# Kernel optimization log

Measured on AMD Instinct MI355X. Metric: run time of the kernel, lower is better.

## Reference

```python
import jax, jax.numpy as jnp
import numpy as np

DIM = 1024
NUM_HEADS = 16
DIM_HEAD = 64
INNER = NUM_HEADS * DIM_HEAD  # 1024
B, N = 2, 2048


def setup_inputs() -> dict:
    key = jax.random.key(0)
    k1, k2, k3 = jax.random.split(key, 3)
    x = jax.random.normal(k1, (B, N, DIM), dtype=jnp.float32)
    # nn.Linear(dim, inner*3, bias=False): weight [3*inner, dim]; y = x @ W^T
    w_qkv = jax.random.normal(k2, (3 * INNER, DIM), dtype=jnp.float32) * (DIM ** -0.5)
    # to_out: Linear(inner, dim) with bias
    w_out = jax.random.normal(k3, (DIM, INNER), dtype=jnp.float32) * (INNER ** -0.5)
    b_out = jnp.zeros((DIM,), dtype=jnp.float32)
    return {"x": x, "w_qkv": w_qkv, "w_out": w_out, "b_out": b_out}


def reference(x, w_qkv, w_out, b_out):
    b, n, d = x.shape
    scale = DIM_HEAD ** -0.5
    qkv = jnp.einsum('bnd,ed->bne', x, w_qkv)  # [b, n, 3*inner]
    q, k, v = jnp.split(qkv, 3, axis=-1)
    # [b, n, h, dh] -> [b, h, n, dh]
    reshape = lambda t: t.reshape(b, n, NUM_HEADS, DIM_HEAD).transpose(0, 2, 1, 3)
    q, k, v = reshape(q), reshape(k), reshape(v)
    dots = jnp.einsum('bhqd,bhkd->bhqk', q, k) * scale  # [b, h, n, n]
    attn = jax.nn.softmax(dots, axis=-1)
    out = jnp.einsum('bhqk,bhkd->bhqd', attn, v)
    out = out.transpose(0, 2, 1, 3).reshape(b, n, INNER)
    out = jnp.einsum('bni,oi->bno', out, w_out) + b_out
    return out
```

## Files before the change

kernel.cpp:

```cpp
#include <hip/hip_runtime.h>
#include <hip/hip_bf16.h>
#include <stdint.h>

typedef unsigned short u16;
typedef short bf16x8 __attribute__((ext_vector_type(8)));
typedef float f32x4 __attribute__((ext_vector_type(4)));
typedef float f32x16 __attribute__((ext_vector_type(16)));
typedef u16 u16x4 __attribute__((ext_vector_type(4)));
typedef unsigned int uint2v __attribute__((ext_vector_type(2)));

#define DIMX  1024
#define NHEAD 16
#define DH    64
#define INNER 1024
#define BATCH 2
#define SEQ   2048
#define MTOT  (BATCH*SEQ)
#define EQKV  (3*INNER)

__device__ __forceinline__ u16 f2bf(float f) {
  unsigned int x = __float_as_uint(f);
  unsigned int r = (x + 0x7FFFu + ((x >> 16) & 1u)) >> 16;
  return (u16)r;
}

__device__ __forceinline__ unsigned int cvtpk(float lo, float hi) {
  unsigned int r;
  asm("v_cvt_pk_bf16_f32 %0, %1, %2" : "=v"(r) : "v"(lo), "v"(hi));
  return r;
}

__device__ __forceinline__ void plswap_u(unsigned int& x, unsigned int& y) {
  auto r = __builtin_amdgcn_permlane32_swap(x, y, false, false);
  x = r[0]; y = r[1];
}
__device__ __forceinline__ void plswap_f2(float v, float& a, float& b) {
  unsigned int x = __float_as_uint(v), y = __float_as_uint(v);
  auto r = __builtin_amdgcn_permlane32_swap(x, y, false, false);
  a = __uint_as_float(r[0]); b = __uint_as_float(r[1]);
}

__device__ __forceinline__ void async16(void* lds, const void* g) {
  __builtin_amdgcn_global_load_lds(
      (const __attribute__((address_space(1))) unsigned int*)g,
      (__attribute__((address_space(3))) unsigned int*)lds,
      16, 0, 0);
}

__device__ __forceinline__ int swz4(int r) { return (r ^ (r >> 2)) & 3; }

#define X4C (MTOT * DIMX / 4)
#define W4C (EQKV * DIMX / 4)
#define O4C (DIMX * INNER / 4)
__global__ void cvt_all(const float* __restrict__ x, const float* __restrict__ wq,
                        const float* __restrict__ wo, u16* __restrict__ xb,
                        u16* __restrict__ wqb, u16* __restrict__ wob) {
  int i = blockIdx.x * blockDim.x + threadIdx.x;
  const float* src; u16* dst; int off;
  if (i < X4C)            { src = x;  dst = xb;  off = i; }
  else if (i < X4C + W4C) { src = wq; dst = wqb; off = i - X4C; }
  else                    { src = wo; dst = wob; off = i - X4C - W4C; }
  float4 v = ((const float4*)src)[off];
  u16x4 o;
  o[0] = f2bf(v.x); o[1] = f2bf(v.y); o[2] = f2bf(v.z); o[3] = f2bf(v.w);
  ((u16x4*)dst)[off] = o;
}

__global__ __launch_bounds__(256) void gemm_qkv(const u16* __restrict__ X, const u16* __restrict__ W,
                                                u16* __restrict__ Qo, u16* __restrict__ Ko,
                                                u16* __restrict__ Vt) {
  __shared__ short sAll[24576];
  short* sA = sAll;
  short* sB = sAll + 12288;
  const int tid = threadIdx.x;
  const int wv = tid >> 6, l = tid & 63;
  const int lo = l & 15, hi = l >> 4;
  const int wr = wv >> 1, wc = wv & 1;

  int lin = blockIdx.x;
  int wgid = (lin & 7) * 96 + (lin >> 3);
  const int bx = wgid / 32;
  const int by = wgid % 32;
  const int tn = bx * 128, tm = by * 128;

  f32x4 acc[4][4];
#pragma unroll
  for (int i = 0; i < 4; i++)
#pragma unroll
    for (int j = 0; j < 4; j++) acc[i][j] = (f32x4){0.f, 0.f, 0.f, 0.f};

  auto stageT = [&](int buf, int kt) {
    int k0 = kt * 32;
    int off = buf * 4096;
#pragma unroll
    for (int c = 0; c < 2; c++) {
      int R0 = wv * 32 + c * 16;
      int r = R0 + (l >> 2);
      int sc = ((l & 3) ^ swz4(r)) * 8;
      async16(&sA[off + R0 * 32], &X[(size_t)(tm + r) * DIMX + k0 + sc]);
      async16(&sB[off + R0 * 32], &W[(size_t)(tn + r) * DIMX + k0 + sc]);
    }
  };

  auto compute = [&](int buf) {
    bf16x8 af[4], bf[4];
#pragma unroll
    for (int i = 0; i < 4; i++) {
      int r = wr * 64 + i * 16 + lo;
      af[i] = *(const bf16x8*)&sA[buf * 4096 + r * 32 + ((hi ^ swz4(r)) * 8)];
    }
#pragma unroll
    for (int j = 0; j < 4; j++) {
      int r = wc * 64 + j * 16 + lo;
      bf[j] = *(const bf16x8*)&sB[buf * 4096 + r * 32 + ((hi ^ swz4(r)) * 8)];
    }
#pragma unroll
    for (int i = 0; i < 4; i++)
#pragma unroll
      for (int j = 0; j < 4; j++)
        acc[i][j] = __builtin_amdgcn_mfma_f32_16x16x32_bf16(af[i], bf[j], acc[i][j], 0, 0, 0);
  };

  const int NT = DIMX / 32;
  stageT(0, 0);
  stageT(1, 1);
  int bc = 0;
  for (int kt = 0; kt < NT - 2; kt++) {
    int bs = bc + 2; if (bs >= 3) bs -= 3;
    stageT(bs, kt + 2);
    asm volatile("s_waitcnt vmcnt(8)" ::: "memory");
    asm volatile("s_barrier" ::: "memory");
    __builtin_amdgcn_sched_barrier(0);
    compute(bc);
    __builtin_amdgcn_sched_barrier(0);
    asm volatile("s_barrier" ::: "memory");
    bc = (bc == 2) ? 0 : bc + 1;
  }
  asm volatile("s_waitcnt vmcnt(4)" ::: "memory");
  asm volatile("s_barrier" ::: "memory");
  __builtin_amdgcn_sched_barrier(0);
  compute(bc);
  __builtin_amdgcn_sched_barrier(0);
  asm volatile("s_barrier" ::: "memory");
  bc = (bc == 2) ? 0 : bc + 1;
  asm volatile("s_waitcnt vmcnt(0)" ::: "memory");
  asm volatile("s_barrier" ::: "memory");
  __builtin_amdgcn_sched_barrier(0);
  compute(bc);
  __builtin_amdgcn_sched_barrier(0);
  __syncthreads();

  const int cls = tn >> 10;
  const float scale = 0.125f * 1.44269504088896f;

  if (cls < 2) {
#pragma unroll
    for (int i = 0; i < 4; i++) {
      int mbase = tm + wr * 64 + i * 16 + hi * 4;
#pragma unroll
      for (int j = 0; j < 4; j++) {
        int e = tn + wc * 64 + j * 16 + lo;
        int e2 = e & 1023, h = e2 >> 6, d = e2 & 63;
        u16* base = (cls == 0) ? Qo : Ko;
        float s = (cls == 0) ? scale : 1.0f;
        size_t a0 = (((size_t)((mbase >> 11) * NHEAD + h)) * SEQ) * DH + d;
#pragma unroll
        for (int rp = 0; rp < 2; rp++) {
          int n0 = (mbase + rp * 2) & 2047;
          unsigned int pk = cvtpk(acc[i][j][rp * 2] * s, acc[i][j][rp * 2 + 1] * s);
          base[a0 + (size_t)n0 * DH] = (u16)pk;
          base[a0 + (size_t)(n0 + 1) * DH] = (u16)(pk >> 16);
        }
      }
    }
  } else {
#pragma unroll
    for (int i = 0; i < 4; i++) {
#pragma unroll
      for (int j = 0; j < 4; j++) {
        int e = wc * 64 + j * 16 + lo;
#pragma unroll
        for (int rp = 0; rp < 2; rp++) {
          int n = wr * 64 + i * 16 + hi * 4 + rp * 2;
          unsigned int pk = cvtpk(acc[i][j][rp * 2], acc[i][j][rp * 2 + 1]);
          *(unsigned int*)&sAll[e * 128 + (((n >> 3) ^ (e & 15)) * 8) + (n & 7)] = pk;
        }
      }
    }
    __syncthreads();
    int er = tid >> 1, half = tid & 1;
    int e2 = tn + er - 2048;
    int h = e2 >> 6, d = e2 & 63;
    int b = tm >> 11, nb = tm & 2047;
    u16* dst = &Vt[(((size_t)(b * NHEAD + h)) * DH + d) * SEQ + nb + half * 64];
#pragma unroll
    for (int k = 0; k < 8; k++) {
      int phys = (half * 8 + k) ^ (er & 15);
      bf16x8 v = *(const bf16x8*)&sAll[er * 128 + phys * 8];
      *(bf16x8*)&dst[k * 8] = v;
    }
  }
}

__global__ __launch_bounds__(256) void attn_kernel(const u16* __restrict__ Q, const u16* __restrict__ Kd,
                                                   const u16* __restrict__ Vt, u16* __restrict__ O) {
  __shared__ short sK[2][64 * 64];
  __shared__ short sV[2][64 * 64];
  const int tid = threadIdx.x, wv = tid >> 6, l = tid & 63;
  const int l31 = l & 31, hi5 = l >> 5, l7 = l & 7;

  int lin = blockIdx.y * gridDim.x + blockIdx.x;
  int wgid = (lin & 7) * 64 + (lin >> 3);
  int bx = wgid & 15;
  int bh = wgid >> 4;

  const int qw = bx * 128 + wv * 32;
  const u16* Qb = Q + (size_t)bh * SEQ * DH;
  const u16* Kb = Kd + (size_t)bh * SEQ * DH;
  const u16* Vb = Vt + (size_t)bh * DH * SEQ;

  bf16x8 qf[4];
#pragma unroll
  for (int kd = 0; kd < 4; kd++)
    qf[kd] = *(const bf16x8*)&Qb[(size_t)(qw + l31) * DH + kd * 16 + hi5 * 8];

  f32x16 o0, o1;
#pragma unroll
  for (int r = 0; r < 16; r++) { o0[r] = 0.f; o1[r] = 0.f; }
  float lsum = 0.f;
  const float CSHIFT = 12.0f;

  auto stage = [&](int buf, int t) {
    int kv0 = t * 64;
#pragma unroll
    for (int c = 0; c < 2; c++) {
      int rbase = wv * 16 + c * 8;
      int gr = rbase + (l >> 3);
      int sc = ((l & 7) ^ (l >> 3)) * 8;
      async16(&sK[buf][rbase * 64], &Kb[(size_t)(kv0 + gr) * DH + sc]);
      async16(&sV[buf][rbase * 64], &Vb[(size_t)gr * SEQ + kv0 + sc]);
    }
  };

  stage(0, 0);
  __syncthreads();

  for (int t = 0; t < SEQ / 64; t++) {
    const int cur = t & 1;
    if (t + 1 < SEQ / 64) stage(cur ^ 1, t + 1);

    bf16x8 kf0[4], kf1[4], vf0[4], vf1[4];
#pragma unroll
    for (int kd = 0; kd < 4; kd++) {
      int c16 = ((kd * 2 + hi5) ^ l7) * 8;
      kf0[kd] = *(const bf16x8*)&sK[cur][l31 * 64 + c16];
      kf1[kd] = *(const bf16x8*)&sK[cur][(32 + l31) * 64 + c16];
      vf0[kd] = *(const bf16x8*)&sV[cur][l31 * 64 + c16];
      vf1[kd] = *(const bf16x8*)&sV[cur][(32 + l31) * 64 + c16];
    }

    f32x16 s0, s1;
#pragma unroll
    for (int r = 0; r < 16; r++) { s0[r] = -CSHIFT; s1[r] = -CSHIFT; }
#pragma unroll
    for (int kd = 0; kd < 4; kd++) {
      s0 = __builtin_amdgcn_mfma_f32_32x32x16_bf16(kf0[kd], qf[kd], s0, 0, 0, 0);
      s1 = __builtin_amdgcn_mfma_f32_32x32x16_bf16(kf1[kd], qf[kd], s1, 0, 0, 0);
    }

    float sm[16];
#pragma unroll
    for (int r = 0; r < 16; r++) {
      s0[r] = __builtin_amdgcn_exp2f(s0[r]);
      s1[r] = __builtin_amdgcn_exp2f(s1[r]);
      sm[r] = s0[r] + s1[r];
    }
#pragma unroll
    for (int st = 8; st > 0; st >>= 1)
#pragma unroll
      for (int r = 0; r < st; r++) sm[r] += sm[r + st];
    lsum += sm[0];

    bf16x8 pa[4];
#pragma unroll
    for (int ks = 0; ks < 4; ks++) {
      const int sft = (ks & 1) * 8;
      float e0 = (ks < 2) ? s0[sft + 0] : s1[sft + 0];
      float e1 = (ks < 2) ? s0[sft + 1] : s1[sft + 1];
      float e2 = (ks < 2) ? s0[sft + 2] : s1[sft + 2];
      float e3 = (ks < 2) ? s0[sft + 3] : s1[sft + 3];
      float e4 = (ks < 2) ? s0[sft + 4] : s1[sft + 4];
      float e5 = (ks < 2) ? s0[sft + 5] : s1[sft + 5];
      float e6 = (ks < 2) ? s0[sft + 6] : s1[sft + 6];
      float e7 = (ks < 2) ? s0[sft + 7] : s1[sft + 7];
      unsigned int w0 = cvtpk(e0, e1);
      unsigned int w1 = cvtpk(e2, e3);
      unsigned int w2 = cvtpk(e4, e5);
      unsigned int w3 = cvtpk(e6, e7);
      plswap_u(w0, w2);
      plswap_u(w1, w3);
      union { unsigned int w[4]; bf16x8 v; } u;
      u.w[0] = w0; u.w[1] = w1; u.w[2] = w2; u.w[3] = w3;
      pa[ks] = u.v;
    }

#pragma unroll
    for (int ks = 0; ks < 4; ks++) {
      o0 = __builtin_amdgcn_mfma_f32_32x32x16_bf16(vf0[ks], pa[ks], o0, 0, 0, 0);
      o1 = __builtin_amdgcn_mfma_f32_32x32x16_bf16(vf1[ks], pa[ks], o1, 0, 0, 0);
    }
    __syncthreads();
  }

  float la, lb;
  plswap_f2(lsum, la, lb);
  float inv = 1.0f / (la + lb);

  int b = bh >> 4, h = bh & 15;
  int q = qw + l31;
  size_t orow = ((size_t)(b * SEQ + q)) * INNER + h * 64;
#pragma unroll
  for (int half = 0; half < 2; half++) {
    const f32x16& oo = half ? o1 : o0;
#pragma unroll
    for (int g = 0; g < 4; g++) {
      uint2v pk2;
      pk2[0] = cvtpk(oo[g * 4 + 0] * inv, oo[g * 4 + 1] * inv);
      pk2[1] = cvtpk(oo[g * 4 + 2] * inv, oo[g * 4 + 3] * inv);
      int dv = half * 32 + g * 8 + 4 * hi5;
      *(uint2v*)&O[orow + dv] = pk2;
    }
  }
}

__global__ __launch_bounds__(256) void gemm_out(const u16* __restrict__ A, const u16* __restrict__ W,
                                                const float* __restrict__ bias, float* __restrict__ out) {
  __shared__ short sAll[12288];
  short* sA = sAll;
  short* sB = sAll + 8192;
  const int tid = threadIdx.x;
  const int wv = tid >> 6, l = tid & 63;
  const int lo = l & 15, hi = l >> 4;
  const int wr = wv >> 1, wc = wv & 1;

  int lin = blockIdx.x;
  int wgid = (lin & 7) * 64 + (lin >> 3);
  const int bx = wgid / 32;
  const int by = wgid % 32;
  const int tn = bx * 64, tm = by * 128;

  f32x4 acc[4][2];
#pragma unroll
  for (int i = 0; i < 4; i++)
#pragma unroll
    for (int j = 0; j < 2; j++) acc[i][j] = (f32x4){0.f, 0.f, 0.f, 0.f};

  auto stage = [&](int buf, int kt) {
    int k0 = kt * 32;
#pragma unroll
    for (int c = 0; c < 2; c++) {
      int R0 = wv * 32 + c * 16;
      int r = R0 + (l >> 2);
      int sc = ((l & 3) ^ swz4(r)) * 8;
      async16(&sA[buf * 4096 + R0 * 32], &A[(size_t)(tm + r) * INNER + k0 + sc]);
    }
    int rB = wv * 16 + (l >> 2);
    int scB = ((l & 3) ^ swz4(rB)) * 8;
    async16(&sB[buf * 2048 + (wv * 16) * 32], &W[(size_t)(tn + rB) * INNER + k0 + scB]);
  };

  stage(0, 0);
  __syncthreads();

  for (int kt = 0; kt < INNER / 32; kt++) {
    const int buf = kt & 1;
    if (kt + 1 < INNER / 32) stage(buf ^ 1, kt + 1);
    bf16x8 af[4], bf[2];
#pragma unroll
    for (int i = 0; i < 4; i++) {
      int r = wr * 64 + i * 16 + lo;
      af[i] = *(const bf16x8*)&sA[buf * 4096 + r * 32 + ((hi ^ swz4(r)) * 8)];
    }
#pragma unroll
    for (int j = 0; j < 2; j++) {
      int r = wc * 32 + j * 16 + lo;
      bf[j] = *(const bf16x8*)&sB[buf * 2048 + r * 32 + ((hi ^ swz4(r)) * 8)];
    }
#pragma unroll
    for (int i = 0; i < 4; i++)
#pragma unroll
      for (int j = 0; j < 2; j++)
        acc[i][j] = __builtin_amdgcn_mfma_f32_16x16x32_bf16(af[i], bf[j], acc[i][j], 0, 0, 0);
    __syncthreads();
  }

#pragma unroll
  for (int i = 0; i < 4; i++) {
    int mbase = tm + wr * 64 + i * 16 + hi * 4;
#pragma unroll
    for (int j = 0; j < 2; j++) {
      int col = tn + wc * 32 + j * 16 + lo;
      float bv = bias[col];
#pragma unroll
      for (int r = 0; r < 4; r++)
        out[(size_t)(mbase + r) * DIMX + col] = acc[i][j][r] + bv;
    }
  }
}

extern "C" void kernel_launch(void* const* d_in, const int* in_sizes, int n_in,
                              void* d_out, int out_size, void* d_ws, size_t ws_size,
                              hipStream_t stream) {
  const float* x     = (const float*)d_in[0];
  const float* w_qkv = (const float*)d_in[1];
  const float* w_out = (const float*)d_in[2];
  const float* b_out = (const float*)d_in[3];

  char* ws = (char*)d_ws;
  u16* xb    = (u16*)(ws);
  u16* wqkvb = (u16*)(ws + (size_t)8  * (1<<20));
  u16* woutb = (u16*)(ws + (size_t)14 * (1<<20));
  u16* Qd    = (u16*)(ws + (size_t)16 * (1<<20));
  u16* Kdd   = (u16*)(ws + (size_t)24 * (1<<20));
  u16* Vtd   = (u16*)(ws + (size_t)32 * (1<<20));
  u16* Od    = (u16*)(ws + (size_t)40 * (1<<20));

  cvt_all<<<(X4C + W4C + O4C) / 256, 256, 0, stream>>>(x, w_qkv, w_out, xb, wqkvb, woutb);

  gemm_qkv<<<768, 256, 0, stream>>>(xb, wqkvb, Qd, Kdd, Vtd);
  attn_kernel<<<dim3(SEQ / 128, BATCH * NHEAD), 256, 0, stream>>>(Qd, Kdd, Vtd, Od);
  gemm_out<<<512, 256, 0, stream>>>(Od, woutb, b_out, (float*)d_out);
}
```

Before: 120.0 us.

## Pre-shuffle K/V into MFMA fragment layout and load directly to registers

The QKV projection epilogue now writes K and V in a layout that matches the per-lane MFMA operand order for each 64-row tile. The attention kernel then loads K and V fragments straight from global memory into registers, with K for the next tile prefetched into a ping-pong register set, instead of staging through LDS with barriers. This removes LDS traffic and the per-tile __syncthreads. In exchange, every wave reads K/V from global/L2 on its own, losing LDS sharing across the 4 waves, and register pressure rises.

```diff
diff --git a/kernel.cpp b/kernel.cpp
--- a/kernel.cpp
+++ b/kernel.cpp
@@ -17,6 +17,8 @@
 #define SEQ   2048
 #define MTOT  (BATCH*SEQ)
 #define EQKV  (3*INNER)
+#define HSTRIDE 131072
+#define TSTRIDE 4096
 
 __device__ __forceinline__ u16 f2bf(float f) {
   unsigned int x = __float_as_uint(f);
@@ -153,23 +155,44 @@
   const int cls = tn >> 10;
   const float scale = 0.125f * 1.44269504088896f;
 
-  if (cls < 2) {
+  if (cls == 0) {
 #pragma unroll
     for (int i = 0; i < 4; i++) {
       int mbase = tm + wr * 64 + i * 16 + hi * 4;
 #pragma unroll
       for (int j = 0; j < 4; j++) {
         int e = tn + wc * 64 + j * 16 + lo;
-        int e2 = e & 1023, h = e2 >> 6, d = e2 & 63;
-        u16* base = (cls == 0) ? Qo : Ko;
-        float s = (cls == 0) ? scale : 1.0f;
+        int h = e >> 6, d = e & 63;
         size_t a0 = (((size_t)((mbase >> 11) * NHEAD + h)) * SEQ) * DH + d;
 #pragma unroll
         for (int rp = 0; rp < 2; rp++) {
           int n0 = (mbase + rp * 2) & 2047;
-          unsigned int pk = cvtpk(acc[i][j][rp * 2] * s, acc[i][j][rp * 2 + 1] * s);
-          base[a0 + (size_t)n0 * DH] = (u16)pk;
-          base[a0 + (size_t)(n0 + 1) * DH] = (u16)(pk >> 16);
+          unsigned int pk = cvtpk(acc[i][j][rp * 2] * scale, acc[i][j][rp * 2 + 1] * scale);
+          Qo[a0 + (size_t)n0 * DH] = (u16)pk;
+          Qo[a0 + (size_t)(n0 + 1) * DH] = (u16)(pk >> 16);
+        }
+      }
+    }
+  } else if (cls == 1) {
+#pragma unroll
+    for (int i = 0; i < 4; i++) {
+      int mbase = tm + wr * 64 + i * 16 + hi * 4;
+      int b = mbase >> 11;
+#pragma unroll
+      for (int j = 0; j < 4; j++) {
+        int e2 = (tn + wc * 64 + j * 16 + lo) - 1024;
+        int h = e2 >> 6, d = e2 & 63;
+        int kd = d >> 4, hi5k = (d >> 3) & 1, e8 = d & 7;
+        size_t hb = (size_t)(b * NHEAD + h) * HSTRIDE + (size_t)kd * 512 + hi5k * 256 + e8;
+#pragma unroll
+        for (int rp = 0; rp < 2; rp++) {
+          int n0 = (mbase + rp * 2) & 2047;
+          int t_ = n0 >> 6, kvi = n0 & 63;
+          int c = kvi >> 5, l31k = kvi & 31;
+          unsigned int pk = cvtpk(acc[i][j][rp * 2], acc[i][j][rp * 2 + 1]);
+          size_t a = hb + (size_t)t_ * TSTRIDE + c * 2048 + l31k * 8;
+          Ko[a] = (u16)pk;
+          Ko[a + 8] = (u16)(pk >> 16);
         }
       }
     }
@@ -190,24 +213,25 @@
     __syncthreads();
     int er = tid >> 1, half = tid & 1;
     int e2 = tn + er - 2048;
-    int h = e2 >> 6, d = e2 & 63;
+    int h = e2 >> 6, dv = e2 & 63;
     int b = tm >> 11, nb = tm & 2047;
-    u16* dst = &Vt[(((size_t)(b * NHEAD + h)) * DH + d) * SEQ + nb + half * 64];
+    int c = dv >> 5, l31v = dv & 31;
+    size_t vb = (size_t)(b * NHEAD + h) * HSTRIDE
+              + (size_t)((nb >> 6) + half) * TSTRIDE + (size_t)c * 2048 + l31v * 8;
 #pragma unroll
     for (int k = 0; k < 8; k++) {
       int phys = (half * 8 + k) ^ (er & 15);
       bf16x8 v = *(const bf16x8*)&sAll[er * 128 + phys * 8];
-      *(bf16x8*)&dst[k * 8] = v;
-    }
-  }
-}
-
-__global__ __launch_bounds__(256) void attn_kernel(const u16* __restrict__ Q, const u16* __restrict__ Kd,
-                                                   const u16* __restrict__ Vt, u16* __restrict__ O) {
-  __shared__ short sK[2][64 * 64];
-  __shared__ short sV[2][64 * 64];
+      int ks = k >> 1, hi5v = k & 1;
+      *(bf16x8*)&Vt[vb + ks * 512 + hi5v * 256] = v;
+    }
+  }
+}
+
+__global__ __launch_bounds__(256) void attn_kernel(const u16* __restrict__ Q, const u16* __restrict__ Ksh,
+                                                   const u16* __restrict__ Vsh, u16* __restrict__ O) {
   const int tid = threadIdx.x, wv = tid >> 6, l = tid & 63;
-  const int l31 = l & 31, hi5 = l >> 5, l7 = l & 7;
+  const int l31 = l & 31, hi5 = l >> 5;
 
   int lin = blockIdx.y * gridDim.x + blockIdx.x;
   int wgid = (lin & 7) * 64 + (lin >> 3);
@@ -216,8 +240,8 @@
 
   const int qw = bx * 128 + wv * 32;
   const u16* Qb = Q + (size_t)bh * SEQ * DH;
-  const u16* Kb = Kd + (size_t)bh * SEQ * DH;
-  const u16* Vb = Vt + (size_t)bh * DH * SEQ;
+  const u16* Kb = Ksh + (size_t)bh * HSTRIDE + l * 8;
+  const u16* Vb = Vsh + (size_t)bh * HSTRIDE + l * 8;
 
   bf16x8 qf[4];
 #pragma unroll
@@ -230,42 +254,35 @@
   float lsum = 0.f;
   const float CSHIFT = 12.0f;
 
-  auto stage = [&](int buf, int t) {
-    int kv0 = t * 64;
-#pragma unroll
-    for (int c = 0; c < 2; c++) {
-      int rbase = wv * 16 + c * 8;
-      int gr = rbase + (l >> 3);
-      int sc = ((l & 7) ^ (l >> 3)) * 8;
-      async16(&sK[buf][rbase * 64], &Kb[(size_t)(kv0 + gr) * DH + sc]);
-      async16(&sV[buf][rbase * 64], &Vb[(size_t)gr * SEQ + kv0 + sc]);
+  bf16x8 kA0[4], kA1[4], kB0[4], kB1[4];
+
+  auto loadK = [&](bf16x8 (&k0)[4], bf16x8 (&k1)[4], int t) {
+    const u16* p = Kb + (size_t)t * TSTRIDE;
+#pragma unroll
+    for (int kd = 0; kd < 4; kd++) {
+      k0[kd] = *(const bf16x8*)&p[kd * 512];
+      k1[kd] = *(const bf16x8*)&p[2048 + kd * 512];
     }
   };
 
-  stage(0, 0);
-  __syncthreads();
-
-  for (int t = 0; t < SEQ / 64; t++) {
-    const int cur = t & 1;
-    if (t + 1 < SEQ / 64) stage(cur ^ 1, t + 1);
-
-    bf16x8 kf0[4], kf1[4], vf0[4], vf1[4];
+  auto tile = [&](bf16x8 (&kc0)[4], bf16x8 (&kc1)[4],
+                  bf16x8 (&kn0)[4], bf16x8 (&kn1)[4], int t) {
+    const u16* pv = Vb + (size_t)t * TSTRIDE;
+    bf16x8 vf0[4], vf1[4];
+#pragma unroll
+    for (int ks = 0; ks < 4; ks++) {
+      vf0[ks] = *(const bf16x8*)&pv[ks * 512];
+      vf1[ks] = *(const bf16x8*)&pv[2048 + ks * 512];
+    }
+    if (t + 1 < SEQ / 64) loadK(kn0, kn1, t + 1);
+
+    f32x16 s0, s1;
+#pragma unroll
+    for (int r = 0; r < 16; r++) { s0[r] = -CSHIFT; s1[r] = -CSHIFT; }
 #pragma unroll
     for (int kd = 0; kd < 4; kd++) {
-      int c16 = ((kd * 2 + hi5) ^ l7) * 8;
-      kf0[kd] = *(const bf16x8*)&sK[cur][l31 * 64 + c16];
-      kf1[kd] = *(const bf16x8*)&sK[cur][(32 + l31) * 64 + c16];
-      vf0[kd] = *(const bf16x8*)&sV[cur][l31 * 64 + c16];
-      vf1[kd] = *(const bf16x8*)&sV[cur][(32 + l31) * 64 + c16];
-    }
-
-    f32x16 s0, s1;
-#pragma unroll
-    for (int r = 0; r < 16; r++) { s0[r] = -CSHIFT; s1[r] = -CSHIFT; }
-#pragma unroll
-    for (int kd = 0; kd < 4; kd++) {
-      s0 = __builtin_amdgcn_mfma_f32_32x32x16_bf16(kf0[kd], qf[kd], s0, 0, 0, 0);
-      s1 = __builtin_amdgcn_mfma_f32_32x32x16_bf16(kf1[kd], qf[kd], s1, 0, 0, 0);
+      s0 = __builtin_amdgcn_mfma_f32_32x32x16_bf16(kc0[kd], qf[kd], s0, 0, 0, 0);
+      s1 = __builtin_amdgcn_mfma_f32_32x32x16_bf16(kc1[kd], qf[kd], s1, 0, 0, 0);
     }
 
     float sm[16];
@@ -309,7 +326,12 @@
       o0 = __builtin_amdgcn_mfma_f32_32x32x16_bf16(vf0[ks], pa[ks], o0, 0, 0, 0);
       o1 = __builtin_amdgcn_mfma_f32_32x32x16_bf16(vf1[ks], pa[ks], o1, 0, 0, 0);
     }
-    __syncthreads();
+  };
+
+  loadK(kA0, kA1, 0);
+  for (int t = 0; t < SEQ / 64; t += 2) {
+    tile(kA0, kA1, kB0, kB1, t);
+    tile(kB0, kB1, kA0, kA1, t + 1);
   }
 
   float la, lb;
```

Measured after the change: 115.9 us, median of 2. -3.4%, faster.
